# Performance work log

Hardware: AMD Instinct MI355X
Metric: run time of the kernel (lower is better)

## Reference

```python
import jax, jax.numpy as jnp
import numpy as np

B, N, DIM, H, DH, M = 2, 2048, 1024, 16, 64, 512
INNER = H * DH  # 1024
KV = M + 1 + N  # xl mem + null kv + sequence = 2561


def rotate_half(x):
    x1, x2 = jnp.split(x, 2, axis=-1)
    return jnp.concatenate([-x2, x1], axis=-1)


def apply_rotary_pos_emb(pos, t):
    return t * jnp.cos(pos) + rotate_half(t) * jnp.sin(pos)


def setup_inputs() -> dict:
    key = jax.random.key(0)
    ks = jax.random.split(key, 8)
    return {
        "x": jax.random.normal(ks[0], (B, N, DIM), jnp.float32),
        "rotary_q": jax.random.uniform(ks[1], (N, DH), jnp.float32) * 6.28,
        "rotary_k": jax.random.uniform(ks[2], (KV, DH), jnp.float32) * 6.28,
        "xl_memories": jax.random.normal(ks[3], (2, B, H, M, DH), jnp.float32) * 0.02,
        "Wq": jax.random.normal(ks[4], (DIM, INNER), jnp.float32) * 0.02,
        "Wkv": jax.random.normal(ks[5], (DIM, 2 * INNER), jnp.float32) * 0.02,
        "Wout": jax.random.normal(ks[6], (INNER, INNER), jnp.float32) * 0.02,
        "null_kv": jax.random.normal(ks[7], (2, H, DH), jnp.float32),
    }


def reference(x, rotary_q, rotary_k, xl_memories, Wq, Wkv, Wout, null_kv):
    # QKV projections (no bias, matching keras Dense(use_bias=False))
    q = (x @ Wq).reshape(B, N, H, DH).transpose(0, 2, 1, 3)  # b h n d
    k, v = jnp.split(x @ Wkv, 2, axis=-1)
    k = k.reshape(B, N, H, DH).transpose(0, 2, 1, 3)
    v = v.reshape(B, N, H, DH).transpose(0, 2, 1, 3)

    # prepend learned null key/value (1 token)
    nk = jnp.broadcast_to(null_kv[0][None, :, None, :], (B, H, 1, DH))
    nv = jnp.broadcast_to(null_kv[1][None, :, None, :], (B, H, 1, DH))
    k = jnp.concatenate([nk, k], axis=2)
    v = jnp.concatenate([nv, v], axis=2)

    next_xl_memories = jnp.stack([k, v])  # [2, b, h, 1+n, d]

    # prepend XL memories along key axis
    k = jnp.concatenate([xl_memories[0], k], axis=2)  # b h kv d
    v = jnp.concatenate([xl_memories[1], v], axis=2)

    # inline rotary embedding on q and (full) k
    q = apply_rotary_pos_emb(rotary_q, q)
    k = apply_rotary_pos_emb(rotary_k, k)

    # causal attention with bottom-right aligned mask (mem/null tokens visible)
    scale = DH ** -0.5
    sim = jnp.einsum('bhid,bhjd->bhij', q, k) * scale  # b h n kv
    i = jnp.arange(N)[:, None]
    j = jnp.arange(KV)[None, :]
    causal_ok = j <= (i + (KV - N))
    sim = jnp.where(causal_ok, sim, jnp.finfo(sim.dtype).min)
    attn = jax.nn.softmax(sim, axis=-1)
    out = jnp.einsum('bhij,bhjd->bhid', attn, v)  # b h n d

    out = out.transpose(0, 2, 1, 3).reshape(B, N, INNER)
    return out @ Wout, next_xl_memories
```

## Files before the change

kernel.cpp:

```cpp
#include <hip/hip_runtime.h>


typedef short v8s __attribute__((ext_vector_type(8)));
typedef float v4f __attribute__((ext_vector_type(4)));

__device__ __forceinline__ float bf2f(unsigned short x) {
  return __uint_as_float(((unsigned)x) << 16);
}
__device__ __forceinline__ unsigned short f2bf(float f) {
  unsigned u = __float_as_uint(f);
  u += 0x7FFFu + ((u >> 16) & 1u);
  return (unsigned short)(u >> 16);
}

#if __has_builtin(__builtin_amdgcn_exp2f)
#define EXP2(x) __builtin_amdgcn_exp2f(x)
#else
#define EXP2(x) exp2f(x)
#endif

template <int CTRL>
__device__ __forceinline__ float dppf(float x) {
  return __int_as_float(
      __builtin_amdgcn_update_dpp(0, __float_as_int(x), CTRL, 0xF, 0xF, true));
}
#define DPP_X1 0xB1
#define DPP_X2 0x4E
#define DPP_X7 0x141
#define DPP_XF 0x140

__device__ __forceinline__ float red_sum16(float v) {
  v += dppf<DPP_X1>(v);
  v += dppf<DPP_X2>(v);
  v += dppf<DPP_X7>(v);
  v += dppf<DPP_XF>(v);
  return v;
}

__device__ __forceinline__ void gld_lds16(const void* g, void* l) {
  __builtin_amdgcn_global_load_lds(
      (const __attribute__((address_space(1))) unsigned int*)g,
      (__attribute__((address_space(3))) unsigned int*)l, 16, 0, 0);
}

__global__ __launch_bounds__(256) void cvt_bf16(
    const float* __restrict__ S, unsigned short* __restrict__ D, int n4)
{
  const int i = blockIdx.x * 256 + threadIdx.x;
  if (i < n4) {
    const float4 v = ((const float4*)S)[i];
    ushort4 o;
    o.x = f2bf(v.x); o.y = f2bf(v.y); o.z = f2bf(v.z); o.w = f2bf(v.w);
    ((ushort4*)D)[i] = o;
  }
}

template <typename CT>
__global__ __launch_bounds__(256, 2) void gemm_bf16(
    const unsigned short* __restrict__ A,
    const unsigned short* __restrict__ WT,
    CT* __restrict__ C,
    int K, int ldc)
{
  __shared__ unsigned short As[128 * 64];
  __shared__ unsigned short Bs[128 * 64];
  const int tid  = threadIdx.x;
  const int wave = tid >> 6, lane = tid & 63;
  const int l15  = lane & 15, quad = lane >> 4;
  const int wm   = wave >> 1, wn = wave & 1;
  const int row0 = blockIdx.x * 128, col0 = blockIdx.y * 128;
  const int lrow = lane >> 3;
  const int gsw  = (lane & 7) ^ lrow;

  v4f acc[4][4];
  const v4f vzero = {0.f, 0.f, 0.f, 0.f};
#pragma unroll
  for (int i = 0; i < 4; ++i)
#pragma unroll
    for (int j = 0; j < 4; ++j) acc[i][j] = vzero;

  for (int k0 = 0; k0 < K; k0 += 64) {
    __syncthreads();
#pragma unroll
    for (int ro = 0; ro < 4; ++ro) {
      const int chunk = wave * 4 + ro;
      const int arow  = chunk * 8 + lrow;
      gld_lds16(A  + (size_t)(row0 + arow) * K + k0 + gsw * 8, As + chunk * 512);
      gld_lds16(WT + (size_t)(col0 + arow) * K + k0 + gsw * 8, Bs + chunk * 512);
    }
    __syncthreads();

    v8s af[4][2], bf[4][2];
#pragma unroll
    for (int tm = 0; tm < 4; ++tm) {
      const int r = wm * 64 + tm * 16 + l15;
#pragma unroll
      for (int kk = 0; kk < 2; ++kk) {
        const int slot = (kk * 4 + quad) ^ (r & 7);
        af[tm][kk] = *(const v8s*)(As + r * 64 + slot * 8);
      }
    }
#pragma unroll
    for (int tn = 0; tn < 4; ++tn) {
      const int r = wn * 64 + tn * 16 + l15;
#pragma unroll
      for (int kk = 0; kk < 2; ++kk) {
        const int slot = (kk * 4 + quad) ^ (r & 7);
        bf[tn][kk] = *(const v8s*)(Bs + r * 64 + slot * 8);
      }
    }
#pragma unroll
    for (int kk = 0; kk < 2; ++kk)
#pragma unroll
      for (int tm = 0; tm < 4; ++tm)
#pragma unroll
        for (int tn = 0; tn < 4; ++tn)
          acc[tm][tn] = __builtin_amdgcn_mfma_f32_16x16x32_bf16(
              af[tm][kk], bf[tn][kk], acc[tm][tn], 0, 0, 0);
  }

#pragma unroll
  for (int tm = 0; tm < 4; ++tm)
#pragma unroll
    for (int tn = 0; tn < 4; ++tn)
#pragma unroll
      for (int r = 0; r < 4; ++r) {
        const int row = row0 + wm * 64 + tm * 16 + quad * 4 + r;
        const int col = col0 + wn * 64 + tn * 16 + l15;
        if constexpr (sizeof(CT) == 2)
          C[(size_t)row * ldc + col] = (CT)f2bf(acc[tm][tn][r]);
        else
          C[(size_t)row * ldc + col] = (CT)acc[tm][tn][r];
      }
}

__global__ __launch_bounds__(256) void transpose_wt(
    const float* __restrict__ S0,
    const float* __restrict__ S1,
    int c0, int c1, int K,
    unsigned short* __restrict__ D)
{
  __shared__ float T[64][65];
  const int k0 = blockIdx.x * 64, n0 = blockIdx.y * 64;
  const int tid = threadIdx.x;
#pragma unroll
  for (int ro = 0; ro < 4; ++ro) {
    const int idx = ro * 256 + tid;
    const int kr = idx >> 4, ch = idx & 15;
    const int n = n0 + ch * 4;
    float4 val;
    if (n < c0) val = *(const float4*)(S0 + (size_t)(k0 + kr) * c0 + n);
    else        val = *(const float4*)(S1 + (size_t)(k0 + kr) * c1 + (n - c0));
    T[kr][ch * 4 + 0] = val.x; T[kr][ch * 4 + 1] = val.y;
    T[kr][ch * 4 + 2] = val.z; T[kr][ch * 4 + 3] = val.w;
  }
  __syncthreads();
#pragma unroll
  for (int ro = 0; ro < 2; ++ro) {
    const int idx = ro * 256 + tid;
    const int nl = idx >> 3, ch = idx & 7;
    __align__(16) unsigned short tmp[8];
#pragma unroll
    for (int e = 0; e < 8; ++e) tmp[e] = f2bf(T[ch * 8 + e][nl]);
    *(uint4*)(D + (size_t)(n0 + nl) * K + k0 + ch * 8) = *(const uint4*)tmp;
  }
}

__global__ __launch_bounds__(256) void assemble(
    const unsigned short* __restrict__ QKV,
    const float* __restrict__ rq,
    const float* __restrict__ rk,
    const float* __restrict__ xlm,
    const float* __restrict__ nkv,
    unsigned short* __restrict__ Qrot,
    unsigned short* __restrict__ Kf,
    unsigned short* __restrict__ Vn,
    float* __restrict__ nxl)
{
  const int gw = blockIdx.x * 4 + (threadIdx.x >> 6);
  const int d  = threadIdx.x & 63;
  const int RK = 32 * 2561;
  if (gw < RK) {
    const int bh = gw / 2561;
    const int j  = gw - bh * 2561;
    const int b  = bh >> 4, h = bh & 15;
    float kx, vx;
    if (j < 512) {
      const size_t i0 = (((size_t)(b * 16 + h)) * 512 + j) * 64 + d;
      kx = xlm[i0];
      vx = xlm[1048576 + i0];
    } else if (j == 512) {
      kx = nkv[h * 64 + d];
      vx = nkv[1024 + h * 64 + d];
    } else {
      const size_t rowb = ((size_t)(b * 2048 + (j - 513))) * 3072;
      kx = bf2f(QKV[rowb + 1024 + h * 64 + d]);
      vx = bf2f(QKV[rowb + 2048 + h * 64 + d]);
    }
    Vn[(((size_t)bh) * 2561 + j) * 64 + d] = f2bf(vx);
    if (j >= 512) {
      const size_t o0 = (((size_t)(b * 16 + h)) * 2049 + (j - 512)) * 64 + d;
      nxl[o0] = kx;
      nxl[4196352 + o0] = vx;
    }
    const float ang = rk[j * 64 + d];
    const float cs = __cosf(ang), sn = __sinf(ang);
    const float part = __shfl_xor(kx, 32);
    const float kr = kx * cs + (d < 32 ? -part : part) * sn;
    Kf[(((size_t)bh) * 2624 + j) * 64 + d] = f2bf(kr);
  } else {
    const int g2 = gw - RK;
    const int bh = g2 >> 11, n = g2 & 2047;
    const int b  = bh >> 4, h = bh & 15;
    const float qx = bf2f(QKV[((size_t)(b * 2048 + n)) * 3072 + h * 64 + d]);
    const float ang = rq[n * 64 + d];
    const float cs = __cosf(ang), sn = __sinf(ang);
    const float part = __shfl_xor(qx, 32);
    const float qr = qx * cs + (d < 32 ? -part : part) * sn;
    Qrot[(((size_t)bh) * 2048 + n) * 64 + d] = f2bf(qr * 0.18033688f);
  }
}

__global__ __launch_bounds__(256) void transpose_v(
    const unsigned short* __restrict__ Vn,
    unsigned short* __restrict__ VTp)
{
  __shared__ unsigned short T[64][72];
  const int j0 = blockIdx.x * 64;
  const int bh = blockIdx.y;
  const int tid = threadIdx.x;
#pragma unroll
  for (int ro = 0; ro < 2; ++ro) {
    const int idx = ro * 256 + tid;
    const int jr = idx >> 3, ch = idx & 7;
    uint4 val = make_uint4(0, 0, 0, 0);
    if (j0 + jr < 2561)
      val = *(const uint4*)(Vn + (((size_t)bh) * 2561 + j0 + jr) * 64 + ch * 8);
    *(uint4*)(&T[jr][ch * 8]) = val;
  }
  __syncthreads();
#pragma unroll
  for (int ro = 0; ro < 2; ++ro) {
    const int idx = ro * 256 + tid;
    const int dl = idx >> 3, ch = idx & 7;
    __align__(16) unsigned short tmp[8];
#pragma unroll
    for (int e = 0; e < 8; ++e) tmp[e] = T[ch * 8 + e][dl];
    *(uint4*)(VTp + (((size_t)bh) * 64 + dl) * 2624 + j0 + ch * 8) = *(const uint4*)tmp;
  }
}

__global__ __launch_bounds__(256, 4) void attn_fa(
    const unsigned short* __restrict__ Qr,
    const unsigned short* __restrict__ Kf,
    const unsigned short* __restrict__ VTp,
    unsigned short* __restrict__ Ao)
{
  const int bh = blockIdx.y;
  const int qb = 31 - (int)((blockIdx.x + blockIdx.y) & 31);
  const int b = bh >> 4, h = bh & 15;
  __shared__ unsigned short QPs[64 * 72];
  __shared__ unsigned short Ks[64 * 72];
  __shared__ unsigned short Vs[64 * 72];
  const int tid = threadIdx.x;
  const int wave = tid >> 6, lane = tid & 63;
  const int l15 = lane & 15, quad = lane >> 4;
  const v4f vzero = {0.f, 0.f, 0.f, 0.f};

  {
    const unsigned short* Qg = Qr + (((size_t)bh) * 2048 + qb * 64) * 64;
#pragma unroll
    for (int ro = 0; ro < 2; ++ro) {
      const int idx = ro * 256 + tid;
      const int row = idx >> 3, ch = idx & 7;
      *(uint4*)(QPs + row * 72 + ch * 8) = *(const uint4*)(Qg + row * 64 + ch * 8);
    }
  }
  __syncthreads();
  v8s qf[2];
  {
    const int r = wave * 16 + l15;
    qf[0] = *(const v8s*)(QPs + r * 72 + quad * 8);
    qf[1] = *(const v8s*)(QPs + r * 72 + 32 + quad * 8);
  }
  unsigned short* Pw = QPs + wave * 16 * 72;

  float l_i[4] = {0.f, 0.f, 0.f, 0.f};
  v4f O[4];
#pragma unroll
  for (int dt = 0; dt < 4; ++dt) O[dt] = vzero;

  const unsigned short* Kg0 = Kf + (size_t)bh * 2624 * 64;
  const unsigned short* Vg0 = VTp + (size_t)bh * 64 * 2624;
  const int ntiles = (qb + 10 <= 41) ? (qb + 10) : 41;
  const int tfast  = qb + 7;

  const int srow = tid >> 3, sch = tid & 7;
  const int srow1 = srow + 32;

#define PREFETCH(t, ka, kb, va, vb)                                          \
  {                                                                          \
    const int j0p = (t) * 64;                                                \
    ka = *(const uint4*)(Kg0 + (size_t)(j0p + srow) * 64 + sch * 8);         \
    va = *(const uint4*)(Vg0 + (size_t)srow * 2624 + j0p + sch * 8);         \
    kb = *(const uint4*)(Kg0 + (size_t)(j0p + srow1) * 64 + sch * 8);        \
    vb = *(const uint4*)(Vg0 + (size_t)srow1 * 2624 + j0p + sch * 8);        \
  }
#define STAGE(ka, kb, va, vb)                                                \
  {                                                                          \
    *(uint4*)(Ks + srow * 72 + sch * 8) = ka;                                \
    *(uint4*)(Vs + srow * 72 + sch * 8) = va;                                \
    *(uint4*)(Ks + srow1 * 72 + sch * 8) = kb;                               \
    *(uint4*)(Vs + srow1 * 72 + sch * 8) = vb;                               \
  }

  auto compute_tile = [&](int j0, bool masked) {
    v4f s[4];
#pragma unroll
    for (int jt = 0; jt < 4; ++jt) {
      const v8s kfr0 = *(const v8s*)(Ks + (jt * 16 + l15) * 72 + quad * 8);
      const v8s kfr1 = *(const v8s*)(Ks + (jt * 16 + l15) * 72 + 32 + quad * 8);
      v4f c = vzero;
      c = __builtin_amdgcn_mfma_f32_16x16x32_bf16(qf[0], kfr0, c, 0, 0, 0);
      c = __builtin_amdgcn_mfma_f32_16x16x32_bf16(qf[1], kfr1, c, 0, 0, 0);
      s[jt] = c;
    }

    if (masked) {
      const int ibase = qb * 64 + wave * 16 + quad * 4 + 513;
#pragma unroll
      for (int jt = 0; jt < 4; ++jt) {
        const int jg = j0 + jt * 16 + l15;
#pragma unroll
        for (int r = 0; r < 4; ++r)
          s[jt][r] = (jg <= ibase + r) ? s[jt][r] : -1e30f;
      }
    }

#pragma unroll
    for (int r = 0; r < 4; ++r) {
      const float p0 = EXP2(s[0][r]);
      const float p1 = EXP2(s[1][r]);
      const float p2 = EXP2(s[2][r]);
      const float p3 = EXP2(s[3][r]);
      l_i[r] += red_sum16(p0 + p1 + p2 + p3);
      const int prow = (quad * 4 + r) * 72 + l15;
      Pw[prow]      = f2bf(p0);
      Pw[prow + 16] = f2bf(p1);
      Pw[prow + 32] = f2bf(p2);
      Pw[prow + 48] = f2bf(p3);
    }
    __asm__ volatile("s_waitcnt lgkmcnt(0)" ::: "memory");

    v8s pf[2];
    pf[0] = *(const v8s*)(Pw + l15 * 72 + quad * 8);
    pf[1] = *(const v8s*)(Pw + l15 * 72 + 32 + quad * 8);
#pragma unroll
    for (int dt = 0; dt < 4; ++dt) {
      const v8s vf0 = *(const v8s*)(Vs + (dt * 16 + l15) * 72 + quad * 8);
      const v8s vf1 = *(const v8s*)(Vs + (dt * 16 + l15) * 72 + 32 + quad * 8);
      v4f c = O[dt];
      c = __builtin_amdgcn_mfma_f32_16x16x32_bf16(pf[0], vf0, c, 0, 0, 0);
      c = __builtin_amdgcn_mfma_f32_16x16x32_bf16(pf[1], vf1, c, 0, 0, 0);
      O[dt] = c;
    }
  };

  uint4 k0a, k0b, v0a, v0b, k1a, k1b, v1a, v1b;
  PREFETCH(0, k0a, k0b, v0a, v0b);
  for (int t = 0; t < ntiles; t += 2) {
    __syncthreads();
    STAGE(k0a, k0b, v0a, v0b);
    if (t + 1 < ntiles) PREFETCH(t + 1, k1a, k1b, v1a, v1b);
    __syncthreads();
    compute_tile(t * 64, t > tfast);
    if (t + 1 >= ntiles) break;
    __syncthreads();
    STAGE(k1a, k1b, v1a, v1b);
    if (t + 2 < ntiles) PREFETCH(t + 2, k0a, k0b, v0a, v0b);
    __syncthreads();
    compute_tile((t + 1) * 64, (t + 1) > tfast);
  }
#undef PREFETCH
#undef STAGE

#pragma unroll
  for (int r = 0; r < 4; ++r) {
    const float linv = 1.0f / l_i[r];
    const int n = qb * 64 + wave * 16 + quad * 4 + r;
    const size_t rowbase = ((size_t)b * 2048 + n) * 1024 + h * 64;
#pragma unroll
    for (int dt = 0; dt < 4; ++dt)
      Ao[rowbase + dt * 16 + l15] = f2bf(O[dt][r] * linv);
  }
}

extern "C" void kernel_launch(void* const* d_in, const int* in_sizes, int n_in,
                              void* d_out, int out_size, void* d_ws, size_t ws_size,
                              hipStream_t stream)
{
  const float* x    = (const float*)d_in[0];
  const float* rq   = (const float*)d_in[1];
  const float* rk   = (const float*)d_in[2];
  const float* xlm  = (const float*)d_in[3];
  const float* Wq   = (const float*)d_in[4];
  const float* Wkv  = (const float*)d_in[5];
  const float* Wout = (const float*)d_in[6];
  const float* nkv  = (const float*)d_in[7];
  float* out = (float*)d_out;
  float* nxl = out + 4194304;
  char* ws = (char*)d_ws;
  unsigned short* QKV   = (unsigned short*)(ws + 0);
  unsigned short* xbf   = (unsigned short*)(ws + 25165824);
  unsigned short* Ao    = (unsigned short*)(ws + 25165824);
  unsigned short* WqkvT = (unsigned short*)(ws + 33554432);
  unsigned short* WoutT = (unsigned short*)(ws + 39845888);
  unsigned short* Qrot  = (unsigned short*)(ws + 41943040);
  unsigned short* Kf    = (unsigned short*)(ws + 50331648);
  unsigned short* Vn    = (unsigned short*)(ws + 61079552);
  unsigned short* VTp   = (unsigned short*)(ws + 71569408);

  cvt_bf16<<<4096, 256, 0, stream>>>(x, xbf, 1048576);
  transpose_wt<<<dim3(16, 48), 256, 0, stream>>>(Wq, Wkv, 1024, 2048, 1024, WqkvT);
  transpose_wt<<<dim3(16, 16), 256, 0, stream>>>(Wout, Wout, 1024, 1024, 1024, WoutT);
  gemm_bf16<unsigned short><<<dim3(32, 24), 256, 0, stream>>>(xbf, WqkvT, QKV, 1024, 3072);
  assemble<<<36872, 256, 0, stream>>>(QKV, rq, rk, xlm, nkv, Qrot, Kf, Vn, nxl);
  transpose_v<<<dim3(41, 32), 256, 0, stream>>>(Vn, VTp);
  attn_fa<<<dim3(32, 32), 256, 0, stream>>>(Qrot, Kf, VTp, Ao);
  gemm_bf16<float><<<dim3(32, 8), 256, 0, stream>>>(Ao, WoutT, out, 1024, 1024);
}
```

Measured before the change: 242.7 us.

## Compute softmax row sums via MFMA and pack P stores with permuted V layout

The per-row softmax denominator is now accumulated with an extra MFMA against a ones vector, replacing the DPP cross-lane reductions. P values are packed two bf16s per 32-bit LDS store, and transpose_v permutes the key order to match the new P layout. Q fragments are loaded directly from global memory, which drops an LDS staging step and a barrier. The assemble kernel also zero-fills the K padding rows so masked padded tiles cannot contribute NaNs. The cost is two extra MFMAs per tile and a more complex index permutation.

```diff
diff --git a/kernel.cpp b/kernel.cpp
--- a/kernel.cpp
+++ b/kernel.cpp
@@ -1,4 +1,5 @@
 #include <hip/hip_runtime.h>
+#include <hip/hip_bf16.h>
 
 
 typedef short v8s __attribute__((ext_vector_type(8)));
@@ -19,28 +20,16 @@
 #define EXP2(x) exp2f(x)
 #endif
 
-template <int CTRL>
-__device__ __forceinline__ float dppf(float x) {
-  return __int_as_float(
-      __builtin_amdgcn_update_dpp(0, __float_as_int(x), CTRL, 0xF, 0xF, true));
-}
-#define DPP_X1 0xB1
-#define DPP_X2 0x4E
-#define DPP_X7 0x141
-#define DPP_XF 0x140
-
-__device__ __forceinline__ float red_sum16(float v) {
-  v += dppf<DPP_X1>(v);
-  v += dppf<DPP_X2>(v);
-  v += dppf<DPP_X7>(v);
-  v += dppf<DPP_XF>(v);
-  return v;
-}
-
 __device__ __forceinline__ void gld_lds16(const void* g, void* l) {
   __builtin_amdgcn_global_load_lds(
       (const __attribute__((address_space(1))) unsigned int*)g,
       (__attribute__((address_space(3))) unsigned int*)l, 16, 0, 0);
+}
+
+__device__ __forceinline__ unsigned pk_bf16(float lo, float hi) {
+  union { __hip_bfloat162 h; unsigned u; } cv;
+  cv.h = __float22bfloat162_rn(make_float2(lo, hi));
+  return cv.u;
 }
 
 __global__ __launch_bounds__(256) void cvt_bf16(
@@ -180,6 +169,7 @@
   const int gw = blockIdx.x * 4 + (threadIdx.x >> 6);
   const int d  = threadIdx.x & 63;
   const int RK = 32 * 2561;
+  const int RQ = 32 * 2048;
   if (gw < RK) {
     const int bh = gw / 2561;
     const int j  = gw - bh * 2561;
@@ -208,7 +198,7 @@
     const float part = __shfl_xor(kx, 32);
     const float kr = kx * cs + (d < 32 ? -part : part) * sn;
     Kf[(((size_t)bh) * 2624 + j) * 64 + d] = f2bf(kr);
-  } else {
+  } else if (gw < RK + RQ) {
     const int g2 = gw - RK;
     const int bh = g2 >> 11, n = g2 & 2047;
     const int b  = bh >> 4, h = bh & 15;
@@ -218,6 +208,11 @@
     const float part = __shfl_xor(qx, 32);
     const float qr = qx * cs + (d < 32 ? -part : part) * sn;
     Qrot[(((size_t)bh) * 2048 + n) * 64 + d] = f2bf(qr * 0.18033688f);
+  } else {
+    const int g3 = gw - RK - RQ;
+    const int bh = g3 / 63;
+    const int jj = 2561 + (g3 - bh * 63);
+    Kf[(((size_t)bh) * 2624 + jj) * 64 + d] = 0;
   }
 }
 
@@ -245,7 +240,11 @@
     const int dl = idx >> 3, ch = idx & 7;
     __align__(16) unsigned short tmp[8];
 #pragma unroll
-    for (int e = 0; e < 8; ++e) tmp[e] = T[ch * 8 + e][dl];
+    for (int e = 0; e < 8; ++e) {
+      const int kappa = ch * 8 + e;
+      const int sig = ((kappa & 31) >> 1) + ((kappa & 1) << 4) + (kappa & 32);
+      tmp[e] = T[sig][dl];
+    }
     *(uint4*)(VTp + (((size_t)bh) * 64 + dl) * 2624 + j0 + ch * 8) = *(const uint4*)tmp;
   }
 }
@@ -259,7 +258,7 @@
   const int bh = blockIdx.y;
   const int qb = 31 - (int)((blockIdx.x + blockIdx.y) & 31);
   const int b = bh >> 4, h = bh & 15;
-  __shared__ unsigned short QPs[64 * 72];
+  __shared__ unsigned short Ps[4 * 16 * 72];
   __shared__ unsigned short Ks[64 * 72];
   __shared__ unsigned short Vs[64 * 72];
   const int tid = threadIdx.x;
@@ -267,28 +266,22 @@
   const int l15 = lane & 15, quad = lane >> 4;
   const v4f vzero = {0.f, 0.f, 0.f, 0.f};
 
-  {
-    const unsigned short* Qg = Qr + (((size_t)bh) * 2048 + qb * 64) * 64;
-#pragma unroll
-    for (int ro = 0; ro < 2; ++ro) {
-      const int idx = ro * 256 + tid;
-      const int row = idx >> 3, ch = idx & 7;
-      *(uint4*)(QPs + row * 72 + ch * 8) = *(const uint4*)(Qg + row * 64 + ch * 8);
-    }
-  }
-  __syncthreads();
   v8s qf[2];
   {
-    const int r = wave * 16 + l15;
-    qf[0] = *(const v8s*)(QPs + r * 72 + quad * 8);
-    qf[1] = *(const v8s*)(QPs + r * 72 + 32 + quad * 8);
-  }
-  unsigned short* Pw = QPs + wave * 16 * 72;
-
-  float l_i[4] = {0.f, 0.f, 0.f, 0.f};
-  v4f O[4];
+    const unsigned short* Qg =
+        Qr + (((size_t)bh) * 2048 + qb * 64 + wave * 16 + l15) * 64;
+    qf[0] = *(const v8s*)(Qg + quad * 8);
+    qf[1] = *(const v8s*)(Qg + 32 + quad * 8);
+  }
+  unsigned short* Pw = Ps + wave * 16 * 72;
+
+  v4f O[4], Ol;
 #pragma unroll
   for (int dt = 0; dt < 4; ++dt) O[dt] = vzero;
+  Ol = vzero;
+  const short one_bf = (short)0x3F80;
+  const v8s ones = {one_bf, one_bf, one_bf, one_bf,
+                    one_bf, one_bf, one_bf, one_bf};
 
   const unsigned short* Kg0 = Kf + (size_t)bh * 2624 * 64;
   const unsigned short* Vg0 = VTp + (size_t)bh * 64 * 2624;
@@ -339,18 +332,14 @@
 
 #pragma unroll
     for (int r = 0; r < 4; ++r) {
-      const float p0 = EXP2(s[0][r]);
-      const float p1 = EXP2(s[1][r]);
-      const float p2 = EXP2(s[2][r]);
-      const float p3 = EXP2(s[3][r]);
-      l_i[r] += red_sum16(p0 + p1 + p2 + p3);
-      const int prow = (quad * 4 + r) * 72 + l15;
-      Pw[prow]      = f2bf(p0);
-      Pw[prow + 16] = f2bf(p1);
-      Pw[prow + 32] = f2bf(p2);
-      Pw[prow + 48] = f2bf(p3);
+      const unsigned d0 = pk_bf16(EXP2(s[0][r]), EXP2(s[1][r]));
+      const unsigned d1 = pk_bf16(EXP2(s[2][r]), EXP2(s[3][r]));
+      unsigned short* pr = Pw + (quad * 4 + r) * 72 + 2 * l15;
+      *(unsigned*)(pr)      = d0;
+      *(unsigned*)(pr + 32) = d1;
     }
     __asm__ volatile("s_waitcnt lgkmcnt(0)" ::: "memory");
+    __builtin_amdgcn_sched_barrier(0);
 
     v8s pf[2];
     pf[0] = *(const v8s*)(Pw + l15 * 72 + quad * 8);
@@ -364,6 +353,8 @@
       c = __builtin_amdgcn_mfma_f32_16x16x32_bf16(pf[1], vf1, c, 0, 0, 0);
       O[dt] = c;
     }
+    Ol = __builtin_amdgcn_mfma_f32_16x16x32_bf16(pf[0], ones, Ol, 0, 0, 0);
+    Ol = __builtin_amdgcn_mfma_f32_16x16x32_bf16(pf[1], ones, Ol, 0, 0, 0);
   };
 
   uint4 k0a, k0b, v0a, v0b, k1a, k1b, v1a, v1b;
@@ -386,7 +377,7 @@
 
 #pragma unroll
   for (int r = 0; r < 4; ++r) {
-    const float linv = 1.0f / l_i[r];
+    const float linv = 1.0f / Ol[r];
     const int n = qb * 64 + wave * 16 + quad * 4 + r;
     const size_t rowbase = ((size_t)b * 2048 + n) * 1024 + h * 64;
 #pragma unroll
@@ -424,7 +415,7 @@
   transpose_wt<<<dim3(16, 48), 256, 0, stream>>>(Wq, Wkv, 1024, 2048, 1024, WqkvT);
   transpose_wt<<<dim3(16, 16), 256, 0, stream>>>(Wout, Wout, 1024, 1024, 1024, WoutT);
   gemm_bf16<unsigned short><<<dim3(32, 24), 256, 0, stream>>>(xbf, WqkvT, QKV, 1024, 3072);
-  assemble<<<36872, 256, 0, stream>>>(QKV, rq, rk, xlm, nkv, Qrot, Kf, Vn, nxl);
+  assemble<<<37376, 256, 0, stream>>>(QKV, rq, rk, xlm, nkv, Qrot, Kf, Vn, nxl);
   transpose_v<<<dim3(41, 32), 256, 0, stream>>>(Vn, VTp);
   attn_fa<<<dim3(32, 32), 256, 0, stream>>>(Qrot, Kf, VTp, Ao);
   gemm_bf16<float><<<dim3(32, 8), 256, 0, stream>>>(Ao, WoutT, out, 1024, 1024);
```

After: 236.9 us. 1.02x faster.
